# Optimization experiments

Hardware: AMD Instinct MI355X
Metric: run time of the kernel (lower is better)

Reference implementation:

```python
import jax, jax.numpy as jnp
import numpy as np
from jax import lax

EPS = 1e-5  # BatchNorm eps (torch default)

def _up2_bilinear_ac(x):
    # bilinear upsample x2, align_corners=True; x: [B,C,H,W]
    B, C, H, W = x.shape
    def axis_interp(n_in, n_out):
        pos = jnp.arange(n_out, dtype=jnp.float32) * ((n_in - 1) / (n_out - 1))
        i0 = jnp.floor(pos).astype(jnp.int32)
        i1 = jnp.minimum(i0 + 1, n_in - 1)
        w = (pos - i0.astype(jnp.float32)).astype(x.dtype)
        return i0, i1, w
    i0, i1, wh = axis_interp(H, 2 * H)
    x = x[:, :, i0, :] * (1.0 - wh)[None, None, :, None] + x[:, :, i1, :] * wh[None, None, :, None]
    j0, j1, ww = axis_interp(W, 2 * W)
    x = x[:, :, :, j0] * (1.0 - ww) + x[:, :, :, j1] * ww
    return x

def setup_inputs() -> dict:
    key = jax.random.key(0)
    ks = jax.random.split(key, 8)
    B, Cin, Cout, H, W = 8, 64, 32, 128, 128
    att, K = 16, 2  # attention_channel = max(int(64*0.0625),16)=16; kernel_num=2
    n = lambda k, s, sc: jax.random.normal(k, s, jnp.float32) * sc
    return {
        'x': n(ks[0], (B, Cin, H, W), 1.0),
        'fc_w': n(ks[1], (att, Cin), 0.1),
        'bn_a_gamma': jnp.ones((att,), jnp.float32), 'bn_a_beta': jnp.zeros((att,), jnp.float32),
        'bn_a_mean': jnp.zeros((att,), jnp.float32), 'bn_a_var': jnp.ones((att,), jnp.float32),
        'ch_w': n(ks[2], (Cin, att), 0.1), 'ch_b': jnp.zeros((Cin,), jnp.float32),
        'fil_w': n(ks[3], (Cout, att), 0.1), 'fil_b': jnp.zeros((Cout,), jnp.float32),
        'sp_w': n(ks[4], (9, att), 0.1), 'sp_b': jnp.zeros((9,), jnp.float32),
        'k_w': n(ks[5], (K, att), 0.1), 'k_b': jnp.zeros((K,), jnp.float32),
        'weight': n(ks[6], (K, Cout, Cin, 3, 3), 0.05),
        'bn_gamma': jnp.ones((Cout,), jnp.float32), 'bn_beta': jnp.zeros((Cout,), jnp.float32),
        'bn_mean': jnp.zeros((Cout,), jnp.float32), 'bn_var': jnp.ones((Cout,), jnp.float32),
    }

def reference(x, fc_w, bn_a_gamma, bn_a_beta, bn_a_mean, bn_a_var,
              ch_w, ch_b, fil_w, fil_b, sp_w, sp_b, k_w, k_b,
              weight, bn_gamma, bn_beta, bn_mean, bn_var):
    x = _up2_bilinear_ac(x)
    B, Cin, H, W = x.shape
    K, Cout = weight.shape[0], weight.shape[1]
    # --- ODConv attention branch (on GAP features) ---
    g = x.mean(axis=(2, 3))                                    # [B,Cin]
    h = g @ fc_w.T                                             # [B,att]
    h = (h - bn_a_mean) / jnp.sqrt(bn_a_var + EPS) * bn_a_gamma + bn_a_beta
    h = jax.nn.relu(h)
    ch_att = jax.nn.sigmoid(h @ ch_w.T + ch_b)                 # [B,Cin]
    fil_att = jax.nn.sigmoid(h @ fil_w.T + fil_b)              # [B,Cout]
    sp_att = jax.nn.sigmoid(h @ sp_w.T + sp_b).reshape(B, 1, 1, 1, 3, 3)
    k_att = jax.nn.softmax(h @ k_w.T + k_b, axis=1).reshape(B, K, 1, 1, 1, 1)
    # per-sample aggregated filters: [B,Cout,Cin,3,3]
    agg_w = jnp.sum(k_att * sp_att * weight[None], axis=1)
    # --- dynamic conv (per-sample filter), channel-attended input ---
    x = x * ch_att[:, :, None, None]
    def conv1(xi, wi):
        return lax.conv_general_dilated(xi[None], wi, (1, 1), [(1, 1), (1, 1)],
                                        dimension_numbers=('NCHW', 'OIHW', 'NCHW'))[0]
    y = jax.vmap(conv1)(x, agg_w)                              # [B,Cout,H,W]
    y = y * fil_att[:, :, None, None]
    # --- BatchNorm2d (inference) + GELU (exact erf) ---
    y = (y - bn_mean[:, None, None]) / jnp.sqrt(bn_var[:, None, None] + EPS)
    y = y * bn_gamma[:, None, None] + bn_beta[:, None, None]
    return jax.nn.gelu(y, approximate=False)
```

## Files before the change

### kernel.cpp

```cpp
#include <hip/hip_runtime.h>
#include <hip/hip_bf16.h>

#define EPSBN 1e-5f

typedef short short8 __attribute__((ext_vector_type(8)));
typedef float f32x16 __attribute__((ext_vector_type(16)));

static __device__ __forceinline__ unsigned short f2u(float f){
  __hip_bfloat16 h = __float2bfloat16(f);
  union { __hip_bfloat16 h; unsigned short u; } c; c.h = h; return c.u;
}

#define WS_G     2048
#define WS_S     7168
#define WS_T     8192
#define WS_AGGB  16384
#define WS_XUP   327680

#define XIN_S 820

__global__ __launch_bounds__(256) void k_up(const float* __restrict__ x,
                                            unsigned int* __restrict__ xup32,
                                            float* __restrict__ g)
{
  __shared__ float xin[16*XIN_S];
  __shared__ float w[128];
  int tid = threadIdx.x;
  int bi  = blockIdx.x;
  int strip = bi & 31, h16 = (bi >> 5) & 3, b = bi >> 7;
  int r0 = strip * 8;
  int i0b = (int)((float)r0 * (127.0f/255.0f));

  if (tid < 128){
    int i = tid;
    float s = 0.f;
    int rstart = max(0, (int)floorf((float)(i-1)*(255.0f/127.0f)));
    #pragma unroll
    for (int k = 0; k < 8; ++k){
      int r = rstart + k;
      if (r <= 255){
        float pos = (float)r * (127.0f/255.0f);
        int i0 = (int)pos; float fr = pos - (float)i0; int i1 = min(i0+1,127);
        if (i0 == i) s += 1.0f - fr;
        if (i1 == i) s += fr;
      }
    }
    w[i] = s;
  }
  for (int e4 = tid; e4 < 3072; e4 += 256){
    int j4 = e4 & 31, ci = (e4 >> 5) & 15, ir = e4 >> 9;
    int row = min(i0b + ir, 127);
    *(float4*)&xin[ci*XIN_S + ir*136 + j4*4] =
      *(const float4*)&x[(((size_t)(b*64 + h16*16 + ci)) << 14) + (row << 7) + j4*4];
  }
  for (int e2 = tid; e2 < 768; e2 += 256){
    int k = e2 & 7, t8 = e2 >> 3;
    int ir = t8 % 6, ci = t8 / 6;
    xin[ci*XIN_S + ir*136 + 128 + k] = 0.f;
  }
  __syncthreads();

  {
    int ci_l = tid >> 4, kk = tid & 15;
    float s = 0.f;
    const float* base = &xin[ci_l*XIN_S];
    #pragma unroll
    for (int row = 0; row < 4; ++row){
      int grow = 4*strip + row;
      int ir = grow - i0b;
      const float* rp = base + ir*136 + kk*8;
      float ss = 0.f;
      #pragma unroll
      for (int j = 0; j < 8; ++j) ss += rp[j]*w[kk*8+j];
      s += w[grow]*ss;
    }
    s += __shfl_down(s, 8, 16);
    s += __shfl_down(s, 4, 16);
    s += __shfl_down(s, 2, 16);
    s += __shfl_down(s, 1, 16);
    if (kk == 0) atomicAdd(&g[b*64 + h16*16 + ci_l], s*(1.0f/65536.0f));
  }

  int ci2 = tid & 7, cbase = tid >> 3;
  const float* b0p = &xin[(ci2*2+0)*XIN_S];
  const float* b1p = &xin[(ci2*2+1)*XIN_S];
  size_t plane32 = ((size_t)(b*4 + h16)) << 19;

  #pragma unroll
  for (int jj = 0; jj < 8; ++jj){
    int c = cbase + 32*jj;
    float pos = (float)c * (127.0f/255.0f);
    int j0 = (int)pos; float ww = pos - (float)j0;

    int irA = 0;
    float A0, B0, A1, B1;
    {
      float x0 = b0p[j0],     x1 = b0p[j0+1];     A0 = x0 + (x1-x0)*ww;
      float y0 = b1p[j0],     y1 = b1p[j0+1];     A1 = y0 + (y1-y0)*ww;
      float x2 = b0p[136+j0], x3 = b0p[136+j0+1]; B0 = x2 + (x3-x2)*ww;
      float y2 = b1p[136+j0], y3 = b1p[136+j0+1]; B1 = y2 + (y3-y2)*ww;
    }
    #pragma unroll
    for (int rr = 0; rr < 8; ++rr){
      int r = r0 + rr;
      float posr = (float)r * (127.0f/255.0f);
      int i0 = (int)posr; float wh = posr - (float)i0;
      int ir0 = i0 - i0b;
      if (ir0 > irA){
        A0 = B0; A1 = B1;
        int irB = ir0 + 1;
        float x0 = b0p[irB*136+j0], x1 = b0p[irB*136+j0+1]; B0 = x0 + (x1-x0)*ww;
        float y0 = b1p[irB*136+j0], y1 = b1p[irB*136+j0+1]; B1 = y0 + (y1-y0)*ww;
        irA = ir0;
      }
      float r0v = A0 + (B0-A0)*wh;
      float r1v = A1 + (B1-A1)*wh;
      unsigned pack = (unsigned)f2u(r0v) | (((unsigned)f2u(r1v)) << 16);
      xup32[plane32 + (size_t)(r*256 + c)*8 + ci2] = pack;
    }
  }
}

__global__ __launch_bounds__(256) void k_aggw(const float* __restrict__ g,
                      const float* __restrict__ fc_w,
                      const float* __restrict__ bga, const float* __restrict__ bba,
                      const float* __restrict__ bma, const float* __restrict__ bva,
                      const float* __restrict__ ch_w, const float* __restrict__ ch_b,
                      const float* __restrict__ fil_w, const float* __restrict__ fil_b,
                      const float* __restrict__ sp_w, const float* __restrict__ sp_b,
                      const float* __restrict__ k_w, const float* __restrict__ k_b,
                      const float* __restrict__ bn_g, const float* __restrict__ bn_b,
                      const float* __restrict__ bn_m, const float* __restrict__ bn_v,
                      const float* __restrict__ weight,
                      unsigned short* __restrict__ aggb,
                      float* __restrict__ sS, float* __restrict__ tT)
{
  __shared__ float h[8][16];
  int tid = threadIdx.x;
  if (tid < 128){
    int b = tid >> 4, a = tid & 15;
    float acc = 0.f;
    for (int c = 0; c < 64; ++c) acc += g[b*64+c] * fc_w[a*64+c];
    float v = (acc - bma[a]) * rsqrtf(bva[a] + EPSBN) * bga[a] + bba[a];
    h[b][a] = fmaxf(v, 0.f);
  }
  __syncthreads();

  int idx = blockIdx.x*256 + tid;
  int ci_l = idx & 31;
  int o    = (idx >> 5) & 31;
  int s    = (idx >> 10) % 9;
  int t2   = (idx >> 10) / 9;
  int cc   = t2 & 1, b = t2 >> 1;
  int ci   = cc*32 + ci_l;

  const float* hb = h[b];
  float zc = ch_b[ci], zs = sp_b[s];
  float z0 = k_b[0],  z1 = k_b[1];
  #pragma unroll
  for (int a = 0; a < 16; ++a){
    float hv = hb[a];
    zc += hv*ch_w[ci*16+a];
    zs += hv*sp_w[s*16+a];
    z0 += hv*k_w[a];
    z1 += hv*k_w[16+a];
  }
  float chv = 1.f/(1.f+expf(-zc));
  float spv = 1.f/(1.f+expf(-zs));
  float m = fmaxf(z0,z1);
  float e0 = expf(z0-m), e1 = expf(z1-m), inv = 1.f/(e0+e1);
  float ka0 = e0*inv, ka1 = e1*inv;
  float w0 = weight[(o*64+ci)*9+s];
  float w1 = weight[((32+o)*64+ci)*9+s];
  aggb[idx] = f2u(chv*spv*(ka0*w0 + ka1*w1));

  if (blockIdx.x == 0){
    int bb = tid >> 5, oo = tid & 31;
    float z = fil_b[oo];
    #pragma unroll
    for (int a = 0; a < 16; ++a) z += h[bb][a]*fil_w[oo*16+a];
    float f = 1.f/(1.f+expf(-z));
    float invs = rsqrtf(bn_v[oo] + EPSBN);
    sS[tid] = f * bn_g[oo] * invs;
    if (bb == 0) tT[oo] = bn_b[oo] - bn_m[oo]*bn_g[oo]*invs;
  }
}

#define XT_STRIDE 40

__global__ __launch_bounds__(256) void k_conv(const unsigned short* __restrict__ xup,
                                              const unsigned short* __restrict__ aggb,
                                              const float* __restrict__ sS,
                                              const float* __restrict__ tT,
                                              float* __restrict__ out)
{
  __shared__ unsigned short xt[18*34*XT_STRIDE];
  __shared__ float sSs[32], tTs[32];

  int tid = threadIdx.x;
  int bi  = blockIdx.x;
  int sw  = ((bi & 7) << 7) + (bi >> 3);
  int b   = sw >> 7, t = sw & 127;
  int p0  = (t >> 3) * 16, q0 = (t & 7) * 32;
  int lane = tid & 63, wv = tid >> 6;
  if (tid < 32){ sSs[tid] = sS[b*32+tid]; tTs[tid] = tT[tid]; }

  f32x16 acc[4];
  #pragma unroll
  for (int i = 0; i < 16; ++i){ acc[0][i]=0.f; acc[1][i]=0.f; acc[2][i]=0.f; acc[3][i]=0.f; }

  int n     = lane & 31;
  int kq    = lane >> 5;
  int rhalf = n >> 4;
  int qb    = n & 15;
  int wrow  = wv * 4;

  const unsigned short* xb0 = xup + (((size_t)(b*4 + 0)) << 20);
  const unsigned short* xb1 = xup + (((size_t)(b*4 + 2)) << 20);
  const short8 zero8 = {0,0,0,0,0,0,0,0};

  short8 pre[10];
  #pragma unroll
  for (int k = 0; k < 10; ++k){
    int e = tid + (k << 8); if (e >= 2448) e -= 2448;
    int rr = e / 136, rem = e - rr*136;
    int qq = rem >> 2, k2 = (rem >> 1) & 1, kqe = rem & 1;
    int gr = p0 - 1 + rr, gq = q0 - 1 + qq;
    bool v = ((unsigned)gr < 256u) && ((unsigned)gq < 256u);
    int ldso = (rr*34 + qq)*XT_STRIDE + k2*16 + kqe*8;
    int pmo  = (k2 << 20) + (gr*256 + gq)*16 + kqe*8;
    short8 cur = zero8; pre[k] = zero8;
    if (v){ cur = *(const short8*)&xb0[pmo]; pre[k] = *(const short8*)&xb1[pmo]; }
    *(short8*)&xt[ldso] = cur;
  }
  __syncthreads();

  auto kloop = [&](const unsigned short* ab){
    short8 a0 = *(const short8*)&ab[0];
    short8 a1 = *(const short8*)&ab[16];
    #pragma unroll
    for (int s = 0; s < 9; ++s){
      int sn = (s < 8) ? s+1 : 8;
      short8 na0 = *(const short8*)&ab[sn*1024];
      short8 na1 = *(const short8*)&ab[sn*1024+16];
      const int ky = s/3, kx = s%3;
      #pragma unroll
      for (int tt = 0; tt < 4; ++tt){
        const int rp = tt >> 1, cb = tt & 1;
        const unsigned short* xrow =
          &xt[((wrow + 2*rp + rhalf + ky)*34 + cb*16 + qb + kx)*XT_STRIDE + kq*8];
        short8 bv0 = *(const short8*)&xrow[0];
        short8 bv1 = *(const short8*)&xrow[16];
        acc[tt] = __builtin_amdgcn_mfma_f32_32x32x16_bf16(a0, bv0, acc[tt], 0, 0, 0);
        acc[tt] = __builtin_amdgcn_mfma_f32_32x32x16_bf16(a1, bv1, acc[tt], 0, 0, 0);
      }
      a0 = na0; a1 = na1;
    }
  };

  kloop(aggb + (size_t)(b*2+0)*9216 + n*32 + kq*8);
  __syncthreads();
  #pragma unroll
  for (int k = 0; k < 10; ++k){
    int e = tid + (k << 8); if (e >= 2448) e -= 2448;
    int rr = e / 136, rem = e - rr*136;
    int qq = rem >> 2, k2 = (rem >> 1) & 1, kqe = rem & 1;
    int ldso = (rr*34 + qq)*XT_STRIDE + k2*16 + kqe*8;
    *(short8*)&xt[ldso] = pre[k];
  }
  __syncthreads();
  kloop(aggb + (size_t)(b*2+1)*9216 + n*32 + kq*8);

  #pragma unroll
  for (int tt = 0; tt < 4; ++tt){
    int rp = tt >> 1, cb = tt & 1;
    int p = p0 + wrow + 2*rp + rhalf;
    int q = q0 + cb*16 + qb;
    #pragma unroll
    for (int r = 0; r < 16; ++r){
      int o = (r & 3) + 8*(r >> 2) + 4*kq;
      float valv = acc[tt][r]*sSs[o] + tTs[o];
      float gl  = 0.5f*valv*(1.f + erff(valv*0.70710678118f));
      out[(((size_t)(b*32+o)) << 16) + (p << 8) + q] = gl;
    }
  }
}

extern "C" void kernel_launch(void* const* d_in, const int* in_sizes, int n_in,
                              void* d_out, int out_size, void* d_ws, size_t ws_size,
                              hipStream_t stream)
{
  const float* x     = (const float*)d_in[0];
  const float* fc_w  = (const float*)d_in[1];
  const float* bga   = (const float*)d_in[2];
  const float* bba   = (const float*)d_in[3];
  const float* bma   = (const float*)d_in[4];
  const float* bva   = (const float*)d_in[5];
  const float* ch_w  = (const float*)d_in[6];
  const float* ch_b  = (const float*)d_in[7];
  const float* fil_w = (const float*)d_in[8];
  const float* fil_b = (const float*)d_in[9];
  const float* sp_w  = (const float*)d_in[10];
  const float* sp_b  = (const float*)d_in[11];
  const float* k_w   = (const float*)d_in[12];
  const float* k_b   = (const float*)d_in[13];
  const float* weight= (const float*)d_in[14];
  const float* bn_g  = (const float*)d_in[15];
  const float* bn_b  = (const float*)d_in[16];
  const float* bn_m  = (const float*)d_in[17];
  const float* bn_v  = (const float*)d_in[18];

  char* ws = (char*)d_ws;
  float* g   = (float*)(ws + WS_G);
  float* sS  = (float*)(ws + WS_S);
  float* tT  = (float*)(ws + WS_T);
  unsigned short* aggb = (unsigned short*)(ws + WS_AGGB);
  unsigned short* xup  = (unsigned short*)(ws + WS_XUP);
  float* out = (float*)d_out;

  hipMemsetAsync(g, 0, 512*sizeof(float), stream);
  hipLaunchKernelGGL(k_up,   dim3(1024), dim3(256), 0, stream, x, (unsigned int*)xup, g);
  hipLaunchKernelGGL(k_aggw, dim3(576),  dim3(256), 0, stream, g, fc_w, bga, bba, bma, bva,
                     ch_w, ch_b, fil_w, fil_b, sp_w, sp_b, k_w, k_b,
                     bn_g, bn_b, bn_m, bn_v, weight, aggb, sS, tT);
  hipLaunchKernelGGL(k_conv, dim3(1024), dim3(256), 0, stream, xup, aggb, sS, tT, out);
}
```

Baseline: 182.2 us.

## Fuse bilinear upsample into conv kernel, stage low-res channel-last source

```diff
diff --git a/kernel.cpp b/kernel.cpp
--- a/kernel.cpp
+++ b/kernel.cpp
@@ -15,21 +15,18 @@
 #define WS_S     7168
 #define WS_T     8192
 #define WS_AGGB  16384
-#define WS_XUP   327680
-
-#define XIN_S 820
-
-__global__ __launch_bounds__(256) void k_up(const float* __restrict__ x,
-                                            unsigned int* __restrict__ xup32,
+#define WS_XSRC  327680
+
+__global__ __launch_bounds__(256) void k_tr(const float* __restrict__ x,
+                                            float* __restrict__ xsrc,
                                             float* __restrict__ g)
 {
-  __shared__ float xin[16*XIN_S];
+  __shared__ float xl[4*16*128];
   __shared__ float w[128];
   int tid = threadIdx.x;
   int bi  = blockIdx.x;
-  int strip = bi & 31, h16 = (bi >> 5) & 3, b = bi >> 7;
-  int r0 = strip * 8;
-  int i0b = (int)((float)r0 * (127.0f/255.0f));
+  int strip = bi & 7, gq = (bi >> 3) & 15, b = bi >> 7;
+  int r0 = strip * 16;
 
   if (tid < 128){
     int i = tid;
@@ -47,77 +44,42 @@
     }
     w[i] = s;
   }
-  for (int e4 = tid; e4 < 3072; e4 += 256){
-    int j4 = e4 & 31, ci = (e4 >> 5) & 15, ir = e4 >> 9;
-    int row = min(i0b + ir, 127);
-    *(float4*)&xin[ci*XIN_S + ir*136 + j4*4] =
-      *(const float4*)&x[(((size_t)(b*64 + h16*16 + ci)) << 14) + (row << 7) + j4*4];
-  }
-  for (int e2 = tid; e2 < 768; e2 += 256){
-    int k = e2 & 7, t8 = e2 >> 3;
-    int ir = t8 % 6, ci = t8 / 6;
-    xin[ci*XIN_S + ir*136 + 128 + k] = 0.f;
-  }
-  __syncthreads();
-
-  {
-    int ci_l = tid >> 4, kk = tid & 15;
-    float s = 0.f;
-    const float* base = &xin[ci_l*XIN_S];
-    #pragma unroll
-    for (int row = 0; row < 4; ++row){
-      int grow = 4*strip + row;
-      int ir = grow - i0b;
-      const float* rp = base + ir*136 + kk*8;
-      float ss = 0.f;
-      #pragma unroll
-      for (int j = 0; j < 8; ++j) ss += rp[j]*w[kk*8+j];
-      s += w[grow]*ss;
-    }
-    s += __shfl_down(s, 8, 16);
-    s += __shfl_down(s, 4, 16);
-    s += __shfl_down(s, 2, 16);
-    s += __shfl_down(s, 1, 16);
-    if (kk == 0) atomicAdd(&g[b*64 + h16*16 + ci_l], s*(1.0f/65536.0f));
-  }
-
-  int ci2 = tid & 7, cbase = tid >> 3;
-  const float* b0p = &xin[(ci2*2+0)*XIN_S];
-  const float* b1p = &xin[(ci2*2+1)*XIN_S];
-  size_t plane32 = ((size_t)(b*4 + h16)) << 19;
-
-  #pragma unroll
-  for (int jj = 0; jj < 8; ++jj){
-    int c = cbase + 32*jj;
-    float pos = (float)c * (127.0f/255.0f);
-    int j0 = (int)pos; float ww = pos - (float)j0;
-
-    int irA = 0;
-    float A0, B0, A1, B1;
-    {
-      float x0 = b0p[j0],     x1 = b0p[j0+1];     A0 = x0 + (x1-x0)*ww;
-      float y0 = b1p[j0],     y1 = b1p[j0+1];     A1 = y0 + (y1-y0)*ww;
-      float x2 = b0p[136+j0], x3 = b0p[136+j0+1]; B0 = x2 + (x3-x2)*ww;
-      float y2 = b1p[136+j0], y3 = b1p[136+j0+1]; B1 = y2 + (y3-y2)*ww;
-    }
-    #pragma unroll
-    for (int rr = 0; rr < 8; ++rr){
-      int r = r0 + rr;
-      float posr = (float)r * (127.0f/255.0f);
-      int i0 = (int)posr; float wh = posr - (float)i0;
-      int ir0 = i0 - i0b;
-      if (ir0 > irA){
-        A0 = B0; A1 = B1;
-        int irB = ir0 + 1;
-        float x0 = b0p[irB*136+j0], x1 = b0p[irB*136+j0+1]; B0 = x0 + (x1-x0)*ww;
-        float y0 = b1p[irB*136+j0], y1 = b1p[irB*136+j0+1]; B1 = y0 + (y1-y0)*ww;
-        irA = ir0;
-      }
-      float r0v = A0 + (B0-A0)*wh;
-      float r1v = A1 + (B1-A1)*wh;
-      unsigned pack = (unsigned)f2u(r0v) | (((unsigned)f2u(r1v)) << 16);
-      xup32[plane32 + (size_t)(r*256 + c)*8 + ci2] = pack;
-    }
+  #pragma unroll
+  for (int k = 0; k < 8; ++k){
+    int n = tid + (k << 8);
+    int ci = n >> 9, r = (n >> 5) & 15, c4 = n & 31;
+    *(float4*)&xl[(ci*16 + r)*128 + c4*4] =
+      *(const float4*)&x[(((size_t)(b*64 + gq*4 + ci)) << 14) + (r0 + r)*128 + c4*4];
+  }
+  __syncthreads();
+
+  float g0=0.f, g1=0.f, g2=0.f, g3=0.f;
+  #pragma unroll
+  for (int k = 0; k < 8; ++k){
+    int m = tid + (k << 8);
+    int r = m >> 7, c = m & 127;
+    float v0 = xl[(0*16 + r)*128 + c];
+    float v1 = xl[(1*16 + r)*128 + c];
+    float v2 = xl[(2*16 + r)*128 + c];
+    float v3 = xl[(3*16 + r)*128 + c];
+    float wt = w[r0 + r] * w[c];
+    g0 += wt*v0; g1 += wt*v1; g2 += wt*v2; g3 += wt*v3;
+    float4 o; o.x = v0; o.y = v1; o.z = v2; o.w = v3;
+    *(float4*)&xsrc[(((((size_t)(b*16 + gq)) << 14) + (size_t)((r0 + r)*128 + c)) << 2)] = o;
+  }
+  #pragma unroll
+  for (int off = 32; off; off >>= 1){
+    g0 += __shfl_down(g0, off);
+    g1 += __shfl_down(g1, off);
+    g2 += __shfl_down(g2, off);
+    g3 += __shfl_down(g3, off);
+  }
+  if ((tid & 63) == 0){
+    const float inv = 1.0f/65536.0f;
+    atomicAdd(&g[b*64 + gq*4 + 0], g0*inv);
+    atomicAdd(&g[b*64 + gq*4 + 1], g1*inv);
+    atomicAdd(&g[b*64 + gq*4 + 2], g2*inv);
+    atomicAdd(&g[b*64 + gq*4 + 3], g3*inv);
   }
 }
 
@@ -188,12 +150,22 @@
 
 #define XT_STRIDE 40
 
-__global__ __launch_bounds__(256) void k_conv(const unsigned short* __restrict__ xup,
+static __device__ __forceinline__ float4 lerp4(float4 a, float4 b, float w){
+  float4 r;
+  r.x = a.x + (b.x - a.x)*w;
+  r.y = a.y + (b.y - a.y)*w;
+  r.z = a.z + (b.z - a.z)*w;
+  r.w = a.w + (b.w - a.w)*w;
+  return r;
+}
+
+__global__ __launch_bounds__(256) void k_conv(const float* __restrict__ xsrc,
                                               const unsigned short* __restrict__ aggb,
                                               const float* __restrict__ sS,
                                               const float* __restrict__ tT,
                                               float* __restrict__ out)
 {
+  __shared__ float srcb[1792*4];
   __shared__ unsigned short xt[18*34*XT_STRIDE];
   __shared__ float sSs[32], tTs[32];
 
@@ -205,6 +177,10 @@
   int lane = tid & 63, wv = tid >> 6;
   if (tid < 32){ sSs[tid] = sS[b*32+tid]; tTs[tid] = tT[tid]; }
 
+  const float SF = 127.0f/255.0f;
+  int i_lo = (int)((float)max(p0-1,0)*SF);
+  int j_lo = (int)((float)max(q0-1,0)*SF);
+
   f32x16 acc[4];
   #pragma unroll
   for (int i = 0; i < 16; ++i){ acc[0][i]=0.f; acc[1][i]=0.f; acc[2][i]=0.f; acc[3][i]=0.f; }
@@ -215,25 +191,63 @@
   int qb    = n & 15;
   int wrow  = wv * 4;
 
-  const unsigned short* xb0 = xup + (((size_t)(b*4 + 0)) << 20);
-  const unsigned short* xb1 = xup + (((size_t)(b*4 + 2)) << 20);
-  const short8 zero8 = {0,0,0,0,0,0,0,0};
-
-  short8 pre[10];
-  #pragma unroll
-  for (int k = 0; k < 10; ++k){
-    int e = tid + (k << 8); if (e >= 2448) e -= 2448;
-    int rr = e / 136, rem = e - rr*136;
-    int qq = rem >> 2, k2 = (rem >> 1) & 1, kqe = rem & 1;
-    int gr = p0 - 1 + rr, gq = q0 - 1 + qq;
-    bool v = ((unsigned)gr < 256u) && ((unsigned)gq < 256u);
-    int ldso = (rr*34 + qq)*XT_STRIDE + k2*16 + kqe*8;
-    int pmo  = (k2 << 20) + (gr*256 + gq)*16 + kqe*8;
-    short8 cur = zero8; pre[k] = zero8;
-    if (v){ cur = *(const short8*)&xb0[pmo]; pre[k] = *(const short8*)&xb1[pmo]; }
-    *(short8*)&xt[ldso] = cur;
-  }
-  __syncthreads();
+  #pragma unroll
+  for (int k = 0; k < 7; ++k){
+    int e = tid + (k << 8);
+    int i = e/160, rem = e - i*160, j = rem >> 3, c = rem & 7;
+    int ig = min(i_lo + i, 127), jg = min(j_lo + j, 127);
+    *(float4*)&srcb[e << 2] =
+      *(const float4*)&xsrc[((((size_t)(b*16 + c)) << 14) + (size_t)(ig*128 + jg)) << 2];
+  }
+  __syncthreads();
+
+  auto interp = [&](){
+    #pragma unroll
+    for (int k = 0; k < 10; ++k){
+      int m = tid + (k << 8); if (m >= 2448) m -= 2448;
+      int cq = m & 7; int tt = m >> 3; int rr = tt/17; int qp = tt - rr*17;
+      int gr = p0 - 1 + rr;
+      int xbase = (rr*34 + 2*qp)*XT_STRIDE + cq*4;
+      bool rv = ((unsigned)gr < 256u);
+      float pos_r = (float)gr * SF;
+      int i0 = (int)pos_r; float wh = pos_r - (float)i0;
+      int io0 = 0, io1 = 0;
+      if (rv){ io0 = i0 - i_lo; io1 = min(i0+1,127) - i_lo; }
+      #pragma unroll
+      for (int cI = 0; cI < 2; ++cI){
+        int gq = q0 - 1 + 2*qp + cI;
+        bool cv = rv && ((unsigned)gq < 256u);
+        float4 v = {0.f,0.f,0.f,0.f};
+        if (cv){
+          float pos_c = (float)gq * SF;
+          int j0 = (int)pos_c; float ww = pos_c - (float)j0;
+          int jo0 = j0 - j_lo, jo1 = min(j0+1,127) - j_lo;
+          float4 c00 = *(const float4*)&srcb[(io0*160 + jo0*8 + cq) << 2];
+          float4 c01 = *(const float4*)&srcb[(io0*160 + jo1*8 + cq) << 2];
+          float4 c10 = *(const float4*)&srcb[(io1*160 + jo0*8 + cq) << 2];
+          float4 c11 = *(const float4*)&srcb[(io1*160 + jo1*8 + cq) << 2];
+          float4 h0 = lerp4(c00, c01, ww);
+          float4 h1 = lerp4(c10, c11, ww);
+          v = lerp4(h0, h1, wh);
+        }
+        unsigned lo = (unsigned)f2u(v.x) | (((unsigned)f2u(v.y)) << 16);
+        unsigned hi = (unsigned)f2u(v.z) | (((unsigned)f2u(v.w)) << 16);
+        uint2 pk; pk.x = lo; pk.y = hi;
+        *(uint2*)&xt[xbase + cI*XT_STRIDE] = pk;
+      }
+    }
+  };
+  interp();
+  __syncthreads();
+
+  float4 pre[7];
+  #pragma unroll
+  for (int k = 0; k < 7; ++k){
+    int e = tid + (k << 8);
+    int i = e/160, rem = e - i*160, j = rem >> 3, c = rem & 7;
+    int ig = min(i_lo + i, 127), jg = min(j_lo + j, 127);
+    pre[k] = *(const float4*)&xsrc[((((size_t)(b*16 + 8 + c)) << 14) + (size_t)(ig*128 + jg)) << 2];
+  }
 
   auto kloop = [&](const unsigned short* ab){
     short8 a0 = *(const short8*)&ab[0];
@@ -261,13 +275,12 @@
   kloop(aggb + (size_t)(b*2+0)*9216 + n*32 + kq*8);
   __syncthreads();
   #pragma unroll
-  for (int k = 0; k < 10; ++k){
-    int e = tid + (k << 8); if (e >= 2448) e -= 2448;
-    int rr = e / 136, rem = e - rr*136;
-    int qq = rem >> 2, k2 = (rem >> 1) & 1, kqe = rem & 1;
-    int ldso = (rr*34 + qq)*XT_STRIDE + k2*16 + kqe*8;
-    *(short8*)&xt[ldso] = pre[k];
-  }
+  for (int k = 0; k < 7; ++k){
+    int e = tid + (k << 8);
+    *(float4*)&srcb[e << 2] = pre[k];
+  }
+  __syncthreads();
+  interp();
   __syncthreads();
   kloop(aggb + (size_t)(b*2+1)*9216 + n*32 + kq*8);
 
@@ -311,17 +324,17 @@
   const float* bn_v  = (const float*)d_in[18];
 
   char* ws = (char*)d_ws;
-  float* g   = (float*)(ws + WS_G);
-  float* sS  = (float*)(ws + WS_S);
-  float* tT  = (float*)(ws + WS_T);
+  float* g    = (float*)(ws + WS_G);
+  float* sS   = (float*)(ws + WS_S);
+  float* tT   = (float*)(ws + WS_T);
   unsigned short* aggb = (unsigned short*)(ws + WS_AGGB);
-  unsigned short* xup  = (unsigned short*)(ws + WS_XUP);
-  float* out = (float*)d_out;
+  float* xsrc = (float*)(ws + WS_XSRC);
+  float* out  = (float*)d_out;
 
   hipMemsetAsync(g, 0, 512*sizeof(float), stream);
-  hipLaunchKernelGGL(k_up,   dim3(1024), dim3(256), 0, stream, x, (unsigned int*)xup, g);
+  hipLaunchKernelGGL(k_tr,   dim3(1024), dim3(256), 0, stream, x, xsrc, g);
   hipLaunchKernelGGL(k_aggw, dim3(576),  dim3(256), 0, stream, g, fc_w, bga, bba, bma, bva,
                      ch_w, ch_b, fil_w, fil_b, sp_w, sp_b, k_w, k_b,
                      bn_g, bn_b, bn_m, bn_v, weight, aggb, sS, tT);
-  hipLaunchKernelGGL(k_conv, dim3(1024), dim3(256), 0, stream, xup, aggb, sS, tT, out);
-}
+  hipLaunchKernelGGL(k_conv, dim3(1024), dim3(256), 0, stream, xsrc, aggb, sS, tT, out);
+}
```

Result: slower. 198.5 us (+9.0%).

## Process two column tiles per conv block with LDS-staged weights and software pipelining

Applied to the files above, without the earlier changes.

```diff
diff --git a/kernel.cpp b/kernel.cpp
--- a/kernel.cpp
+++ b/kernel.cpp
@@ -4,6 +4,7 @@
 #define EPSBN 1e-5f
 
 typedef short short8 __attribute__((ext_vector_type(8)));
+typedef short short4v __attribute__((ext_vector_type(4)));
 typedef float f32x16 __attribute__((ext_vector_type(16)));
 
 static __device__ __forceinline__ unsigned short f2u(float f){
@@ -187,6 +188,7 @@
 }
 
 #define XT_STRIDE 40
+#define AG_STRIDE 36
 
 __global__ __launch_bounds__(256) void k_conv(const unsigned short* __restrict__ xup,
                                               const unsigned short* __restrict__ aggb,
@@ -195,55 +197,79 @@
                                               float* __restrict__ out)
 {
   __shared__ unsigned short xt[18*34*XT_STRIDE];
+  __shared__ unsigned short agA[9*32*AG_STRIDE];
   __shared__ float sSs[32], tTs[32];
 
   int tid = threadIdx.x;
   int bi  = blockIdx.x;
-  int sw  = ((bi & 7) << 7) + (bi >> 3);
-  int b   = sw >> 7, t = sw & 127;
-  int p0  = (t >> 3) * 16, q0 = (t & 7) * 32;
+  int sw  = ((bi & 7) << 6) + (bi >> 3);
+  int b   = sw >> 6, t6 = sw & 63;
+  int p0  = (t6 >> 2) * 16;
+  int qA  = (t6 & 3) * 64;
   int lane = tid & 63, wv = tid >> 6;
   if (tid < 32){ sSs[tid] = sS[b*32+tid]; tTs[tid] = tT[tid]; }
+
+  int n = lane & 31, kq = lane >> 5;
+  int rhalf = n >> 4, qb = n & 15, wrow = wv*4;
+
+  const short8 zero8 = {0,0,0,0,0,0,0,0};
+  const unsigned short* xbase = xup + (((size_t)(b*4)) << 20);
+  const unsigned int*   agg32 = (const unsigned int*)(aggb + (size_t)(b*2)*9216);
 
   f32x16 acc[4];
   #pragma unroll
   for (int i = 0; i < 16; ++i){ acc[0][i]=0.f; acc[1][i]=0.f; acc[2][i]=0.f; acc[3][i]=0.f; }
 
-  int n     = lane & 31;
-  int kq    = lane >> 5;
-  int rhalf = n >> 4;
-  int qb    = n & 15;
-  int wrow  = wv * 4;
-
-  const unsigned short* xb0 = xup + (((size_t)(b*4 + 0)) << 20);
-  const unsigned short* xb1 = xup + (((size_t)(b*4 + 2)) << 20);
-  const short8 zero8 = {0,0,0,0,0,0,0,0};
-
-  short8 pre[10];
-  #pragma unroll
-  for (int k = 0; k < 10; ++k){
-    int e = tid + (k << 8); if (e >= 2448) e -= 2448;
-    int rr = e / 136, rem = e - rr*136;
-    int qq = rem >> 2, k2 = (rem >> 1) & 1, kqe = rem & 1;
-    int gr = p0 - 1 + rr, gq = q0 - 1 + qq;
-    bool v = ((unsigned)gr < 256u) && ((unsigned)gq < 256u);
-    int ldso = (rr*34 + qq)*XT_STRIDE + k2*16 + kqe*8;
-    int pmo  = (k2 << 20) + (gr*256 + gq)*16 + kqe*8;
-    short8 cur = zero8; pre[k] = zero8;
-    if (v){ cur = *(const short8*)&xb0[pmo]; pre[k] = *(const short8*)&xb1[pmo]; }
-    *(short8*)&xt[ldso] = cur;
-  }
-  __syncthreads();
-
-  auto kloop = [&](const unsigned short* ab){
-    short8 a0 = *(const short8*)&ab[0];
-    short8 a1 = *(const short8*)&ab[16];
+  short8 cur[10];
+  unsigned int ar[18];
+
+  auto loadx = [&](int q0, int cc){
+    const unsigned short* xb = xbase + (((size_t)(cc*2)) << 20);
+    #pragma unroll
+    for (int k = 0; k < 10; ++k){
+      int e = tid + (k << 8); if (e >= 2448) e -= 2448;
+      int rr = e / 136, rem = e - rr*136;
+      int qq = rem >> 2, k2 = (rem >> 1) & 1, kqe = rem & 1;
+      int gr = p0 - 1 + rr, gq = q0 - 1 + qq;
+      bool v = ((unsigned)gr < 256u) && ((unsigned)gq < 256u);
+      cur[k] = zero8;
+      if (v) cur[k] = *(const short8*)&xb[(k2 << 20) + (gr*256 + gq)*16 + kqe*8];
+    }
+  };
+  auto commitx = [&](){
+    #pragma unroll
+    for (int k = 0; k < 10; ++k){
+      int e = tid + (k << 8); if (e >= 2448) e -= 2448;
+      int rr = e / 136, rem = e - rr*136;
+      int qq = rem >> 2, k2 = (rem >> 1) & 1, kqe = rem & 1;
+      *(short8*)&xt[(rr*34 + qq)*XT_STRIDE + k2*16 + kqe*8] = cur[k];
+    }
+  };
+  auto loada = [&](int cc){
+    const unsigned int* s = agg32 + cc*4608;
+    #pragma unroll
+    for (int k = 0; k < 18; ++k) ar[k] = s[tid + (k << 8)];
+  };
+  auto commita = [&](){
+    unsigned int* d32 = (unsigned int*)agA;
+    #pragma unroll
+    for (int k = 0; k < 18; ++k){
+      int e = tid + (k << 8);
+      int c2 = e & 15, nn = (e >> 4) & 31, s = e >> 9;
+      d32[s*(32*(AG_STRIDE/2)) + nn*(AG_STRIDE/2) + c2] = ar[k];
+    }
+  };
+
+  auto kloop = [&](){
     #pragma unroll
     for (int s = 0; s < 9; ++s){
-      int sn = (s < 8) ? s+1 : 8;
-      short8 na0 = *(const short8*)&ab[sn*1024];
-      short8 na1 = *(const short8*)&ab[sn*1024+16];
-      const int ky = s/3, kx = s%3;
+      const unsigned short* arow = &agA[(s*32 + n)*AG_STRIDE + kq*8];
+      short8 a0, a1;
+      *(short4v*)&a0        = *(const short4v*)&arow[0];
+      *(((short4v*)&a0)+1)  = *(const short4v*)&arow[4];
+      *(short4v*)&a1        = *(const short4v*)&arow[16];
+      *(((short4v*)&a1)+1)  = *(const short4v*)&arow[20];
+      const int ky = s/3, kx = s - ky*3;
       #pragma unroll
       for (int tt = 0; tt < 4; ++tt){
         const int rp = tt >> 1, cb = tt & 1;
@@ -254,36 +280,48 @@
         acc[tt] = __builtin_amdgcn_mfma_f32_32x32x16_bf16(a0, bv0, acc[tt], 0, 0, 0);
         acc[tt] = __builtin_amdgcn_mfma_f32_32x32x16_bf16(a1, bv1, acc[tt], 0, 0, 0);
       }
-      a0 = na0; a1 = na1;
-    }
-  };
-
-  kloop(aggb + (size_t)(b*2+0)*9216 + n*32 + kq*8);
-  __syncthreads();
+    }
+  };
+
+  auto epi = [&](int q0){
+    #pragma unroll
+    for (int tt = 0; tt < 4; ++tt){
+      int rp = tt >> 1, cb = tt & 1;
+      int p = p0 + wrow + 2*rp + rhalf;
+      int q = q0 + cb*16 + qb;
+      #pragma unroll
+      for (int r = 0; r < 16; ++r){
+        int o = (r & 3) + 8*(r >> 2) + 4*kq;
+        float valv = acc[tt][r]*sSs[o] + tTs[o];
+        out[(((size_t)(b*32+o)) << 16) + (p << 8) + q] =
+          0.5f*valv*(1.f + erff(valv*0.70710678118f));
+      }
+    }
+  };
+
+  loadx(qA, 0); loada(0);
+  commitx(); commita();
+  loadx(qA, 1); loada(1);
+  __syncthreads();
+  kloop();
+  __syncthreads();
+  commitx(); commita();
+  loadx(qA+32, 1);
+  __syncthreads();
+  kloop();
+  epi(qA);
   #pragma unroll
-  for (int k = 0; k < 10; ++k){
-    int e = tid + (k << 8); if (e >= 2448) e -= 2448;
-    int rr = e / 136, rem = e - rr*136;
-    int qq = rem >> 2, k2 = (rem >> 1) & 1, kqe = rem & 1;
-    int ldso = (rr*34 + qq)*XT_STRIDE + k2*16 + kqe*8;
-    *(short8*)&xt[ldso] = pre[k];
-  }
-  __syncthreads();
-  kloop(aggb + (size_t)(b*2+1)*9216 + n*32 + kq*8);
-
-  #pragma unroll
-  for (int tt = 0; tt < 4; ++tt){
-    int rp = tt >> 1, cb = tt & 1;
-    int p = p0 + wrow + 2*rp + rhalf;
-    int q = q0 + cb*16 + qb;
-    #pragma unroll
-    for (int r = 0; r < 16; ++r){
-      int o = (r & 3) + 8*(r >> 2) + 4*kq;
-      float valv = acc[tt][r]*sSs[o] + tTs[o];
-      float gl  = 0.5f*valv*(1.f + erff(valv*0.70710678118f));
-      out[(((size_t)(b*32+o)) << 16) + (p << 8) + q] = gl;
-    }
-  }
+  for (int i = 0; i < 16; ++i){ acc[0][i]=0.f; acc[1][i]=0.f; acc[2][i]=0.f; acc[3][i]=0.f; }
+  __syncthreads();
+  commitx();
+  loadx(qA+32, 0); loada(0);
+  __syncthreads();
+  kloop();
+  __syncthreads();
+  commitx(); commita();
+  __syncthreads();
+  kloop();
+  epi(qA+32);
 }
 
 extern "C" void kernel_launch(void* const* d_in, const int* in_sizes, int n_in,
@@ -323,5 +361,5 @@
   hipLaunchKernelGGL(k_aggw, dim3(576),  dim3(256), 0, stream, g, fc_w, bga, bba, bma, bva,
                      ch_w, ch_b, fil_w, fil_b, sp_w, sp_b, k_w, k_b,
                      bn_g, bn_b, bn_m, bn_v, weight, aggb, sS, tT);
-  hipLaunchKernelGGL(k_conv, dim3(1024), dim3(256), 0, stream, xup, aggb, sS, tT, out);
-}
+  hipLaunchKernelGGL(k_conv, dim3(512),  dim3(256), 0, stream, xup, aggb, sS, tT, out);
+}
```

Result: slower. 213.6 us (+17.3%).
